# Kernel tuning notes

Measured on AMD Instinct MI355X. Metric: run time of the kernel, lower is better.

The kernel has to match this reference:

```python
import jax, jax.numpy as jnp
import numpy as np
import math

HEAD_DIM = 128

def _rope(t, cos, sin):
    # t: [B, S, H, D]; cos/sin: [S, D//2]; rotates consecutive pairs (view_as_complex semantics)
    B, S, H, D = t.shape
    t2 = t.reshape(B, S, H, D // 2, 2)
    t0, t1 = t2[..., 0], t2[..., 1]
    c = cos[None, :, None, :]
    s = sin[None, :, None, :]
    r0 = t0 * c - t1 * s
    r1 = t0 * s + t1 * c
    return jnp.stack([r0, r1], axis=-1).reshape(B, S, H, D)

def setup_inputs() -> dict:
    key = jax.random.key(0)
    ks = jax.random.split(key, 8)
    B, S, dim = 32, 1, 4096
    n_q, n_kv, hd = 32, 8, HEAD_DIM
    max_seq = 2048
    start_pos = 2047
    x = jax.random.normal(ks[0], (B, S, dim), dtype=jnp.float32)
    wq = jax.random.normal(ks[1], (n_q * hd, dim), dtype=jnp.float32) * 0.02
    wk = jax.random.normal(ks[2], (n_kv * hd, dim), dtype=jnp.float32) * 0.02
    wv = jax.random.normal(ks[3], (n_kv * hd, dim), dtype=jnp.float32) * 0.02
    wo = jax.random.normal(ks[4], (dim, n_q * hd), dtype=jnp.float32) * 0.02
    # real RoPE frequencies at positions [start_pos, start_pos+S)
    inv_freq = 1.0 / (10000.0 ** (np.arange(0, hd, 2, dtype=np.float32) / hd))  # [hd//2]
    pos = np.arange(start_pos, start_pos + S, dtype=np.float32)[:, None]
    angles = pos * inv_freq[None, :]  # [S, hd//2]
    freqs_cos = jnp.asarray(np.cos(angles), dtype=jnp.float32)
    freqs_sin = jnp.asarray(np.sin(angles), dtype=jnp.float32)
    cache_k = jax.random.normal(ks[5], (B, max_seq, n_kv, hd), dtype=jnp.float32)
    cache_v = jax.random.normal(ks[6], (B, max_seq, n_kv, hd), dtype=jnp.float32)
    return {"x": x, "wq": wq, "wk": wk, "wv": wv, "wo": wo,
            "freqs_cos": freqs_cos, "freqs_sin": freqs_sin,
            "cache_k": cache_k, "cache_v": cache_v, "start_pos": start_pos}

def reference(x, wq, wk, wv, wo, freqs_cos, freqs_sin, cache_k, cache_v, start_pos):
    B, S, dim = x.shape
    hd = HEAD_DIM
    n_q = wq.shape[0] // hd
    n_kv = wk.shape[0] // hd
    rep = n_q // n_kv
    q = (x @ wq.T).reshape(B, S, n_q, hd)
    k = (x @ wk.T).reshape(B, S, n_kv, hd)
    v = (x @ wv.T).reshape(B, S, n_kv, hd)
    q = _rope(q, freqs_cos, freqs_sin)
    k = _rope(k, freqs_cos, freqs_sin)
    # KV-cache update (start_pos is a static Python int)
    ck = jax.lax.dynamic_update_slice(cache_k, k, (0, start_pos, 0, 0))
    cv = jax.lax.dynamic_update_slice(cache_v, v, (0, start_pos, 0, 0))
    T = start_pos + S
    kk = ck[:, :T]  # [B, T, n_kv, hd]
    vv = cv[:, :T]
    # GQA without materializing repeated heads: q head h -> (g=h//rep, r=h%rep)
    qg = q.reshape(B, S, n_kv, rep, hd)
    scores = jnp.einsum('bsgrd,btgd->bgrst', qg, kk) / math.sqrt(hd)
    attn = jax.nn.softmax(scores, axis=-1)
    out = jnp.einsum('bgrst,btgd->bsgrd', attn, vv).reshape(B, S, n_q * hd)
    return out @ wo.T
```

## Files before the change

kernel.cpp:

```cpp
#include <hip/hip_runtime.h>
#include <hip/hip_bf16.h>


typedef __bf16 bf16x8_t __attribute__((ext_vector_type(8)));
typedef float f32x4_t __attribute__((ext_vector_type(4)));

#define KDIM 4096
#define NTOT_QKV 6144
#define NTOT_O 4096
#define NKV 8
#define HD 128

static __device__ inline bf16x8_t cvt8r(float4 u, float4 v) {
  bf16x8_t r;
  r[0] = (__bf16)u.x; r[1] = (__bf16)u.y; r[2] = (__bf16)u.z; r[3] = (__bf16)u.w;
  r[4] = (__bf16)v.x; r[5] = (__bf16)v.y; r[6] = (__bf16)v.z; r[7] = (__bf16)v.w;
  return r;
}

__global__ __launch_bounds__(256) void cast_x(const float* __restrict__ X,
                                              __bf16* __restrict__ Xb) {
  int i = blockIdx.x * 256 + threadIdx.x;
  const float4* p = (const float4*)(X + (size_t)i * 8);
  *(bf16x8_t*)(Xb + (size_t)i * 8) = cvt8r(p[0], p[1]);
}

__global__ __launch_bounds__(256) void qkv_mfma(
    const __bf16* __restrict__ Xb,
    const float* __restrict__ Wq,
    const float* __restrict__ Wk,
    const float* __restrict__ Wv,
    float* __restrict__ part)
{
  int nt = blockIdx.x % 96;
  int kc = blockIdx.x / 96;
  int k0 = kc << 9;
  int tid = threadIdx.x;
  int w = tid >> 6, lane = tid & 63;
  int rr = lane & 15, quad = lane >> 4;

  int ngbase = nt * 64;
  const float* Wbase;
  if (nt < 64)      Wbase = Wq + (size_t)ngbase * KDIM;
  else if (nt < 80) Wbase = Wk + (size_t)(ngbase - 4096) * KDIM;
  else              Wbase = Wv + (size_t)(ngbase - 5120) * KDIM;

  __shared__ bf16x8_t wl[2][512];

  int f8a = tid, f8b = tid + 256;
  int ra = f8a >> 3, ca = f8a & 7;
  int rb = f8b >> 3, cb = f8b & 7;
  const float4* ga = (const float4*)(Wbase + (size_t)ra * KDIM + k0 + ca * 8);
  const float4* gb = (const float4*)(Wbase + (size_t)rb * KDIM + k0 + cb * 8);
  int sa = ra * 8 + (ca ^ (ra & 7));
  int sb = rb * 8 + (cb ^ (rb & 7));

  const __bf16* xa0 = Xb + (size_t)rr * KDIM + k0 + quad * 8;
  const __bf16* xa1 = Xb + (size_t)(rr + 16) * KDIM + k0 + quad * 8;
  int brow = w * 16 + rr;
  int bs0 = brow * 8 + ((quad)     ^ (brow & 7));
  int bs1 = brow * 8 + ((quad + 4) ^ (brow & 7));

  f32x4_t acc0 = {0.f, 0.f, 0.f, 0.f};
  f32x4_t acc1 = {0.f, 0.f, 0.f, 0.f};

  float4 wa0 = ga[0], wa1 = ga[1], wb0 = gb[0], wb1 = gb[1];
  bf16x8_t A00 = *(const bf16x8_t*)(xa0);
  bf16x8_t A10 = *(const bf16x8_t*)(xa1);
  bf16x8_t A01 = *(const bf16x8_t*)(xa0 + 32);
  bf16x8_t A11 = *(const bf16x8_t*)(xa1 + 32);
  wl[0][sa] = cvt8r(wa0, wa1);
  wl[0][sb] = cvt8r(wb0, wb1);
  __syncthreads();

  #pragma unroll
  for (int s = 0; s < 8; ++s) {
    int cur = s & 1;
    float4 nwa0, nwa1, nwb0, nwb1;
    bf16x8_t N00, N10, N01, N11;
    if (s < 7) {
      nwa0 = ga[(s + 1) * 16];     nwa1 = ga[(s + 1) * 16 + 1];
      nwb0 = gb[(s + 1) * 16];     nwb1 = gb[(s + 1) * 16 + 1];
      N00 = *(const bf16x8_t*)(xa0 + (s + 1) * 64);
      N10 = *(const bf16x8_t*)(xa1 + (s + 1) * 64);
      N01 = *(const bf16x8_t*)(xa0 + (s + 1) * 64 + 32);
      N11 = *(const bf16x8_t*)(xa1 + (s + 1) * 64 + 32);
    }
    bf16x8_t b0 = wl[cur][bs0];
    bf16x8_t b1 = wl[cur][bs1];
    acc0 = __builtin_amdgcn_mfma_f32_16x16x32_bf16(A00, b0, acc0, 0, 0, 0);
    acc1 = __builtin_amdgcn_mfma_f32_16x16x32_bf16(A10, b0, acc1, 0, 0, 0);
    acc0 = __builtin_amdgcn_mfma_f32_16x16x32_bf16(A01, b1, acc0, 0, 0, 0);
    acc1 = __builtin_amdgcn_mfma_f32_16x16x32_bf16(A11, b1, acc1, 0, 0, 0);
    if (s < 7) {
      wl[cur ^ 1][sa] = cvt8r(nwa0, nwa1);
      wl[cur ^ 1][sb] = cvt8r(nwb0, nwb1);
      A00 = N00; A10 = N10; A01 = N01; A11 = N11;
    }
    __syncthreads();
  }

  int ng = ngbase + w * 16 + rr;
  float* p = part + (size_t)kc * 32 * NTOT_QKV + ng;
  #pragma unroll
  for (int i = 0; i < 4; ++i) {
    int m = quad * 4 + i;
    p[(size_t)m * NTOT_QKV] = acc0[i];
    p[(size_t)(m + 16) * NTOT_QKV] = acc1[i];
  }
}

__global__ __launch_bounds__(256) void reduce_rope(
    const float* __restrict__ part,
    const float* __restrict__ cosv,
    const float* __restrict__ sinv,
    float* __restrict__ qws,
    float* __restrict__ kws,
    float* __restrict__ vws)
{
  int idx = blockIdx.x * blockDim.x + threadIdx.x;
  int b = idx / 3072;
  int rem = idx - b * 3072;
  int n0 = rem * 2;
  const float* p = part + (size_t)b * NTOT_QKV + n0;
  float s0 = 0.f, s1 = 0.f;
  #pragma unroll
  for (int c = 0; c < 8; ++c) {
    s0 += p[(size_t)c * 32 * NTOT_QKV + 0];
    s1 += p[(size_t)c * 32 * NTOT_QKV + 1];
  }
  if (n0 < 4096) {
    int d = n0 & 127; int j = d >> 1;
    float cf = cosv[j], sf = sinv[j];
    qws[(size_t)b * 4096 + n0]     = s0 * cf - s1 * sf;
    qws[(size_t)b * 4096 + n0 + 1] = s0 * sf + s1 * cf;
  } else if (n0 < 5120) {
    int nn = n0 - 4096;
    int d = nn & 127; int j = d >> 1;
    float cf = cosv[j], sf = sinv[j];
    kws[(size_t)b * 1024 + nn]     = s0 * cf - s1 * sf;
    kws[(size_t)b * 1024 + nn + 1] = s0 * sf + s1 * cf;
  } else {
    int nn = n0 - 5120;
    vws[(size_t)b * 1024 + nn]     = s0;
    vws[(size_t)b * 1024 + nn + 1] = s1;
  }
}

__global__ __launch_bounds__(256) void attn_partial(
    const float* __restrict__ cache_k,
    const float* __restrict__ cache_v,
    const float* __restrict__ qws,
    const float* __restrict__ kws,
    const float* __restrict__ vws,
    float* __restrict__ part)
{
  int bidx = blockIdx.x;
  int c = bidx & 7;
  int pair = bidx >> 3;
  int h = pair & 7, b = pair >> 3;
  int tid = threadIdx.x;

  __shared__ float4 kbuf[2048];
  __shared__ float4 q4l[128];
  __shared__ float4 pl4[256];

  if (tid < 128)
    q4l[tid] = ((const float4*)(qws + (size_t)b * 4096 + (size_t)h * 512))[tid];

  const int r  = tid >> 6;
  const int tl = tid & 63;
  const int sw = tl & 7;

  const float* kcb = cache_k + (((size_t)b * 2048 + c * 256) * NKV + h) * HD;
  const float4* knew = (const float4*)(kws + ((size_t)b * NKV + h) * HD);

  float4 tmp[8];
  #pragma unroll
  for (int j = 0; j < 8; ++j) {
    int f = tid + j * 256, row = f >> 5, col = f & 31;
    tmp[j] = *((const float4*)(kcb + (size_t)row * (NKV * HD)) + col);
  }

  float s[4];
  #pragma unroll
  for (int st = 0; st < 4; ++st) {
    #pragma unroll
    for (int j = 0; j < 8; ++j) {
      int f = tid + j * 256;
      int row = f >> 5, col = f & 31;
      kbuf[row * 32 + (col ^ (row & 7))] = tmp[j];
    }
    __syncthreads();
    if (st < 3) {
      #pragma unroll
      for (int j = 0; j < 8; ++j) {
        int f = tid + j * 256, row = f >> 5, col = f & 31;
        const float4* src;
        if (c == 7 && st == 2 && row == 63)
          src = knew + col;
        else
          src = (const float4*)(kcb + (size_t)((st + 1) * 64 + row) * (NKV * HD)) + col;
        tmp[j] = *src;
      }
    }
    const float4* kr = kbuf + tl * 32;
    float acc = 0.f;
    #pragma unroll 8
    for (int d4 = 0; d4 < 32; ++d4) {
      float4 q4 = q4l[r * 32 + d4];
      float4 k4 = kr[d4 ^ sw];
      acc += q4.x * k4.x + q4.y * k4.y + q4.z * k4.z + q4.w * k4.w;
    }
    s[st] = acc * 0.088388347648318447f;
    __syncthreads();
  }

  float m = fmaxf(fmaxf(s[0], s[1]), fmaxf(s[2], s[3]));
  #pragma unroll
  for (int off = 32; off; off >>= 1) m = fmaxf(m, __shfl_xor(m, off, 64));
  float lsum = 0.f;
  float* plf = (float*)pl4;
  #pragma unroll
  for (int st = 0; st < 4; ++st) {
    float p = __expf(s[st] - m);
    lsum += p;
    plf[(st * 64 + tl) * 4 + r] = p;
  }
  #pragma unroll
  for (int off = 32; off; off >>= 1) lsum += __shfl_xor(lsum, off, 64);

  float* pb = part + (size_t)bidx * 520;
  if (tl == 0) { pb[r] = m; pb[4 + r] = lsum; }
  __syncthreads();

  int d4 = tid & 31;
  int g  = tid >> 5;
  float4 a0 = {0,0,0,0}, a1 = {0,0,0,0}, a2 = {0,0,0,0}, a3 = {0,0,0,0};
  const float4* vp = (const float4*)(cache_v +
      (((size_t)b * 2048 + c * 256 + g * 32) * NKV + h) * HD) + d4;
  #pragma unroll 4
  for (int i = 0; i < 32; ++i) {
    float4 v4 = vp[(size_t)i * 256];
    float4 pv = pl4[g * 32 + i];
    a0.x += pv.x * v4.x; a0.y += pv.x * v4.y; a0.z += pv.x * v4.z; a0.w += pv.x * v4.w;
    a1.x += pv.y * v4.x; a1.y += pv.y * v4.y; a1.z += pv.y * v4.z; a1.w += pv.y * v4.w;
    a2.x += pv.z * v4.x; a2.y += pv.z * v4.y; a2.z += pv.z * v4.z; a2.w += pv.z * v4.w;
    a3.x += pv.w * v4.x; a3.y += pv.w * v4.y; a3.z += pv.w * v4.z; a3.w += pv.w * v4.w;
  }
  if (c == 7 && g == 7) {
    float4 vold = vp[(size_t)31 * 256];
    float4 vn = ((const float4*)(vws + ((size_t)b * NKV + h) * HD))[d4];
    float4 dv; dv.x = vn.x - vold.x; dv.y = vn.y - vold.y;
    dv.z = vn.z - vold.z; dv.w = vn.w - vold.w;
    float4 pv = pl4[255];
    a0.x += pv.x * dv.x; a0.y += pv.x * dv.y; a0.z += pv.x * dv.z; a0.w += pv.x * dv.w;
    a1.x += pv.y * dv.x; a1.y += pv.y * dv.y; a1.z += pv.y * dv.z; a1.w += pv.y * dv.w;
    a2.x += pv.z * dv.x; a2.y += pv.z * dv.y; a2.z += pv.z * dv.z; a2.w += pv.z * dv.w;
    a3.x += pv.w * dv.x; a3.y += pv.w * dv.y; a3.z += pv.w * dv.z; a3.w += pv.w * dv.w;
  }
  float4* pred = kbuf;
  pred[(g * 4 + 0) * 32 + d4] = a0;
  pred[(g * 4 + 1) * 32 + d4] = a1;
  pred[(g * 4 + 2) * 32 + d4] = a2;
  pred[(g * 4 + 3) * 32 + d4] = a3;
  __syncthreads();

  if (tid < 128) {
    int r2 = tid >> 5, dd = tid & 31;
    float4 o = {0,0,0,0};
    #pragma unroll
    for (int gg = 0; gg < 8; ++gg) {
      float4 t4 = pred[(gg * 4 + r2) * 32 + dd];
      o.x += t4.x; o.y += t4.y; o.z += t4.z; o.w += t4.w;
    }
    *(float4*)(pb + 8 + r2 * 128 + dd * 4) = o;
  }
}

__global__ __launch_bounds__(128) void attn_combine(
    const float* __restrict__ part,
    __bf16* __restrict__ aobf)
{
  int pair = blockIdx.x;
  int h = pair & 7, b = pair >> 3;
  int d = threadIdx.x;
  const float* pb = part + (size_t)pair * 8 * 520;
  #pragma unroll
  for (int r = 0; r < 4; ++r) {
    float M = -1e30f;
    #pragma unroll
    for (int c = 0; c < 8; ++c) M = fmaxf(M, pb[c * 520 + r]);
    float L = 0.f, o = 0.f;
    #pragma unroll
    for (int c = 0; c < 8; ++c) {
      float w = __expf(pb[c * 520 + r] - M);
      L += w * pb[c * 520 + 4 + r];
      o += w * pb[c * 520 + 8 + r * 128 + d];
    }
    aobf[(size_t)b * 4096 + (h * 4 + r) * 128 + d] = (__bf16)(o / L);
  }
}

__global__ __launch_bounds__(256) void oproj_mfma(
    const __bf16* __restrict__ Xb,
    const float* __restrict__ W,
    float* __restrict__ part)
{
  int nt = blockIdx.x & 63;
  int kc = blockIdx.x >> 6;
  int k0 = kc << 9;
  int tid = threadIdx.x;
  int w = tid >> 6, lane = tid & 63;
  int rr = lane & 15, quad = lane >> 4;

  int ngbase = nt * 64;
  const float* Wbase = W + (size_t)ngbase * KDIM;

  __shared__ bf16x8_t wl[2][512];

  int f8a = tid, f8b = tid + 256;
  int ra = f8a >> 3, ca = f8a & 7;
  int rb = f8b >> 3, cb = f8b & 7;
  const float4* ga = (const float4*)(Wbase + (size_t)ra * KDIM + k0 + ca * 8);
  const float4* gb = (const float4*)(Wbase + (size_t)rb * KDIM + k0 + cb * 8);
  int sa = ra * 8 + (ca ^ (ra & 7));
  int sb = rb * 8 + (cb ^ (rb & 7));

  const __bf16* xa0 = Xb + (size_t)rr * KDIM + k0 + quad * 8;
  const __bf16* xa1 = Xb + (size_t)(rr + 16) * KDIM + k0 + quad * 8;
  int brow = w * 16 + rr;
  int bs0 = brow * 8 + ((quad)     ^ (brow & 7));
  int bs1 = brow * 8 + ((quad + 4) ^ (brow & 7));

  f32x4_t acc0 = {0.f, 0.f, 0.f, 0.f};
  f32x4_t acc1 = {0.f, 0.f, 0.f, 0.f};

  float4 wa0 = ga[0], wa1 = ga[1], wb0 = gb[0], wb1 = gb[1];
  bf16x8_t A00 = *(const bf16x8_t*)(xa0);
  bf16x8_t A10 = *(const bf16x8_t*)(xa1);
  bf16x8_t A01 = *(const bf16x8_t*)(xa0 + 32);
  bf16x8_t A11 = *(const bf16x8_t*)(xa1 + 32);
  wl[0][sa] = cvt8r(wa0, wa1);
  wl[0][sb] = cvt8r(wb0, wb1);
  __syncthreads();

  #pragma unroll
  for (int s = 0; s < 8; ++s) {
    int cur = s & 1;
    float4 nwa0, nwa1, nwb0, nwb1;
    bf16x8_t N00, N10, N01, N11;
    if (s < 7) {
      nwa0 = ga[(s + 1) * 16];     nwa1 = ga[(s + 1) * 16 + 1];
      nwb0 = gb[(s + 1) * 16];     nwb1 = gb[(s + 1) * 16 + 1];
      N00 = *(const bf16x8_t*)(xa0 + (s + 1) * 64);
      N10 = *(const bf16x8_t*)(xa1 + (s + 1) * 64);
      N01 = *(const bf16x8_t*)(xa0 + (s + 1) * 64 + 32);
      N11 = *(const bf16x8_t*)(xa1 + (s + 1) * 64 + 32);
    }
    bf16x8_t b0 = wl[cur][bs0];
    bf16x8_t b1 = wl[cur][bs1];
    acc0 = __builtin_amdgcn_mfma_f32_16x16x32_bf16(A00, b0, acc0, 0, 0, 0);
    acc1 = __builtin_amdgcn_mfma_f32_16x16x32_bf16(A10, b0, acc1, 0, 0, 0);
    acc0 = __builtin_amdgcn_mfma_f32_16x16x32_bf16(A01, b1, acc0, 0, 0, 0);
    acc1 = __builtin_amdgcn_mfma_f32_16x16x32_bf16(A11, b1, acc1, 0, 0, 0);
    if (s < 7) {
      wl[cur ^ 1][sa] = cvt8r(nwa0, nwa1);
      wl[cur ^ 1][sb] = cvt8r(nwb0, nwb1);
      A00 = N00; A10 = N10; A01 = N01; A11 = N11;
    }
    __syncthreads();
  }

  int ng = ngbase + w * 16 + rr;
  float* p = part + (size_t)kc * 32 * NTOT_O + ng;
  #pragma unroll
  for (int i = 0; i < 4; ++i) {
    int m = quad * 4 + i;
    p[(size_t)m * NTOT_O] = acc0[i];
    p[(size_t)(m + 16) * NTOT_O] = acc1[i];
  }
}

__global__ __launch_bounds__(256) void oproj_reduce(
    const float* __restrict__ part,
    float* __restrict__ out)
{
  int i = blockIdx.x * blockDim.x + threadIdx.x;
  float s = 0.f;
  #pragma unroll
  for (int c = 0; c < 8; ++c) s += part[(size_t)c * 131072 + i];
  out[i] = s;
}

extern "C" void kernel_launch(void* const* d_in, const int* in_sizes, int n_in,
                              void* d_out, int out_size, void* d_ws, size_t ws_size,
                              hipStream_t stream) {
  const float* x  = (const float*)d_in[0];
  const float* wq = (const float*)d_in[1];
  const float* wk = (const float*)d_in[2];
  const float* wv = (const float*)d_in[3];
  const float* wo = (const float*)d_in[4];
  const float* fc = (const float*)d_in[5];
  const float* fs = (const float*)d_in[6];
  const float* ck = (const float*)d_in[7];
  const float* cv = (const float*)d_in[8];

  char* ws = (char*)d_ws;
  float*  part_qkv = (float*)(ws + 0);
  float*  qws      = (float*)(ws + 6291456);
  float*  kws      = (float*)(ws + 6815744);
  float*  vws      = (float*)(ws + 6946816);
  float*  part_at  = (float*)(ws + 7077888);
  __bf16* xbf      = (__bf16*)(ws + 11337728);
  __bf16* aobf     = (__bf16*)(ws + 11599872);
  float*  part_o   = (float*)(ws + 0);

  cast_x<<<64, 256, 0, stream>>>(x, xbf);
  qkv_mfma<<<768, 256, 0, stream>>>(xbf, wq, wk, wv, part_qkv);
  reduce_rope<<<384, 256, 0, stream>>>(part_qkv, fc, fs, qws, kws, vws);
  attn_partial<<<2048, 256, 0, stream>>>(ck, cv, qws, kws, vws, part_at);
  attn_combine<<<256, 128, 0, stream>>>(part_at, aobf);
  oproj_mfma<<<512, 256, 0, stream>>>(aobf, wo, part_o);
  oproj_reduce<<<512, 256, 0, stream>>>(part_o, (float*)d_out);
}
```

Baseline: 678.3 us.

## Compute attention scores straight from global K, dropping LDS K staging

The QK^T phase no longer stages 256 K rows through a 32KB shared buffer with double-buffered register prefetch and barriers. Each group of 4 lanes now reads one K row directly from global memory and reduces partial dots with shuffles, with q held in registers. Shared memory drops to about 20KB and launch bounds request 4 blocks per CU, aiming for more occupancy and no barriers in the score loop. The cost is that each of the 4 warps reads the same K rows redundantly, relying on cache for reuse, and every lane redoes the exp, so the row sum is scaled by 0.25.

Measured after the change: 678.6 us. About the same (+0.1%).

```diff
diff --git a/kernel.cpp b/kernel.cpp
--- a/kernel.cpp
+++ b/kernel.cpp
@@ -147,7 +147,7 @@
   }
 }
 
-__global__ __launch_bounds__(256) void attn_partial(
+__global__ __launch_bounds__(256, 4) void attn_partial(
     const float* __restrict__ cache_k,
     const float* __restrict__ cache_v,
     const float* __restrict__ qws,
@@ -161,74 +161,57 @@
   int h = pair & 7, b = pair >> 3;
   int tid = threadIdx.x;
 
-  __shared__ float4 kbuf[2048];
-  __shared__ float4 q4l[128];
-  __shared__ float4 pl4[256];
-
-  if (tid < 128)
-    q4l[tid] = ((const float4*)(qws + (size_t)b * 4096 + (size_t)h * 512))[tid];
+  __shared__ float plf[4 * 256];
+  __shared__ float4 pred[1024];
 
   const int r  = tid >> 6;
   const int tl = tid & 63;
-  const int sw = tl & 7;
+  const int tq = tl >> 2;
+  const int dq = tl & 3;
+
+  const float4* Q4 = (const float4*)(qws + (size_t)b * 4096 + (size_t)h * 512) + r * 32;
+  float4 q4[8];
+  #pragma unroll
+  for (int i = 0; i < 8; ++i) q4[i] = Q4[dq + 4 * i];
 
   const float* kcb = cache_k + (((size_t)b * 2048 + c * 256) * NKV + h) * HD;
   const float4* knew = (const float4*)(kws + ((size_t)b * NKV + h) * HD);
 
-  float4 tmp[8];
-  #pragma unroll
-  for (int j = 0; j < 8; ++j) {
-    int f = tid + j * 256, row = f >> 5, col = f & 31;
-    tmp[j] = *((const float4*)(kcb + (size_t)row * (NKV * HD)) + col);
-  }
-
-  float s[4];
-  #pragma unroll
-  for (int st = 0; st < 4; ++st) {
+  float sreg[16];
+  #pragma unroll
+  for (int ps = 0; ps < 16; ++ps) {
+    int trow = ps * 16 + tq;
+    const float4* kp = (c == 7 && trow == 255)
+        ? knew
+        : (const float4*)(kcb + (size_t)trow * (NKV * HD));
+    float acc = 0.f;
     #pragma unroll
-    for (int j = 0; j < 8; ++j) {
-      int f = tid + j * 256;
-      int row = f >> 5, col = f & 31;
-      kbuf[row * 32 + (col ^ (row & 7))] = tmp[j];
-    }
-    __syncthreads();
-    if (st < 3) {
-      #pragma unroll
-      for (int j = 0; j < 8; ++j) {
-        int f = tid + j * 256, row = f >> 5, col = f & 31;
-        const float4* src;
-        if (c == 7 && st == 2 && row == 63)
-          src = knew + col;
-        else
-          src = (const float4*)(kcb + (size_t)((st + 1) * 64 + row) * (NKV * HD)) + col;
-        tmp[j] = *src;
-      }
-    }
-    const float4* kr = kbuf + tl * 32;
-    float acc = 0.f;
-    #pragma unroll 8
-    for (int d4 = 0; d4 < 32; ++d4) {
-      float4 q4 = q4l[r * 32 + d4];
-      float4 k4 = kr[d4 ^ sw];
-      acc += q4.x * k4.x + q4.y * k4.y + q4.z * k4.z + q4.w * k4.w;
-    }
-    s[st] = acc * 0.088388347648318447f;
-    __syncthreads();
-  }
-
-  float m = fmaxf(fmaxf(s[0], s[1]), fmaxf(s[2], s[3]));
+    for (int i = 0; i < 8; ++i) {
+      float4 k4 = kp[dq + 4 * i];
+      float4 qq = q4[i];
+      acc += qq.x * k4.x + qq.y * k4.y + qq.z * k4.z + qq.w * k4.w;
+    }
+    acc += __shfl_xor(acc, 1, 64);
+    acc += __shfl_xor(acc, 2, 64);
+    sreg[ps] = acc * 0.088388347648318447f;
+  }
+
+  float m = sreg[0];
+  #pragma unroll
+  for (int ps = 1; ps < 16; ++ps) m = fmaxf(m, sreg[ps]);
   #pragma unroll
   for (int off = 32; off; off >>= 1) m = fmaxf(m, __shfl_xor(m, off, 64));
+
   float lsum = 0.f;
-  float* plf = (float*)pl4;
-  #pragma unroll
-  for (int st = 0; st < 4; ++st) {
-    float p = __expf(s[st] - m);
+  #pragma unroll
+  for (int ps = 0; ps < 16; ++ps) {
+    float p = __expf(sreg[ps] - m);
     lsum += p;
-    plf[(st * 64 + tl) * 4 + r] = p;
+    if (dq == 0) plf[r * 256 + ps * 16 + tq] = p;
   }
   #pragma unroll
   for (int off = 32; off; off >>= 1) lsum += __shfl_xor(lsum, off, 64);
+  lsum *= 0.25f;
 
   float* pb = part + (size_t)bidx * 520;
   if (tl == 0) { pb[r] = m; pb[4 + r] = lsum; }
@@ -242,24 +225,30 @@
   #pragma unroll 4
   for (int i = 0; i < 32; ++i) {
     float4 v4 = vp[(size_t)i * 256];
-    float4 pv = pl4[g * 32 + i];
-    a0.x += pv.x * v4.x; a0.y += pv.x * v4.y; a0.z += pv.x * v4.z; a0.w += pv.x * v4.w;
-    a1.x += pv.y * v4.x; a1.y += pv.y * v4.y; a1.z += pv.y * v4.z; a1.w += pv.y * v4.w;
-    a2.x += pv.z * v4.x; a2.y += pv.z * v4.y; a2.z += pv.z * v4.z; a2.w += pv.z * v4.w;
-    a3.x += pv.w * v4.x; a3.y += pv.w * v4.y; a3.z += pv.w * v4.z; a3.w += pv.w * v4.w;
+    int t = g * 32 + i;
+    float p0 = plf[t];
+    float p1 = plf[256 + t];
+    float p2 = plf[512 + t];
+    float p3 = plf[768 + t];
+    a0.x += p0 * v4.x; a0.y += p0 * v4.y; a0.z += p0 * v4.z; a0.w += p0 * v4.w;
+    a1.x += p1 * v4.x; a1.y += p1 * v4.y; a1.z += p1 * v4.z; a1.w += p1 * v4.w;
+    a2.x += p2 * v4.x; a2.y += p2 * v4.y; a2.z += p2 * v4.z; a2.w += p2 * v4.w;
+    a3.x += p3 * v4.x; a3.y += p3 * v4.y; a3.z += p3 * v4.z; a3.w += p3 * v4.w;
   }
   if (c == 7 && g == 7) {
     float4 vold = vp[(size_t)31 * 256];
     float4 vn = ((const float4*)(vws + ((size_t)b * NKV + h) * HD))[d4];
     float4 dv; dv.x = vn.x - vold.x; dv.y = vn.y - vold.y;
     dv.z = vn.z - vold.z; dv.w = vn.w - vold.w;
-    float4 pv = pl4[255];
-    a0.x += pv.x * dv.x; a0.y += pv.x * dv.y; a0.z += pv.x * dv.z; a0.w += pv.x * dv.w;
-    a1.x += pv.y * dv.x; a1.y += pv.y * dv.y; a1.z += pv.y * dv.z; a1.w += pv.y * dv.w;
-    a2.x += pv.z * dv.x; a2.y += pv.z * dv.y; a2.z += pv.z * dv.z; a2.w += pv.z * dv.w;
-    a3.x += pv.w * dv.x; a3.y += pv.w * dv.y; a3.z += pv.w * dv.z; a3.w += pv.w * dv.w;
-  }
-  float4* pred = kbuf;
+    float p0 = plf[255];
+    float p1 = plf[256 + 255];
+    float p2 = plf[512 + 255];
+    float p3 = plf[768 + 255];
+    a0.x += p0 * dv.x; a0.y += p0 * dv.y; a0.z += p0 * dv.z; a0.w += p0 * dv.w;
+    a1.x += p1 * dv.x; a1.y += p1 * dv.y; a1.z += p1 * dv.z; a1.w += p1 * dv.w;
+    a2.x += p2 * dv.x; a2.y += p2 * dv.y; a2.z += p2 * dv.z; a2.w += p2 * dv.w;
+    a3.x += p3 * dv.x; a3.y += p3 * dv.y; a3.z += p3 * dv.z; a3.w += p3 * dv.w;
+  }
   pred[(g * 4 + 0) * 32 + d4] = a0;
   pred[(g * 4 + 1) * 32 + d4] = a1;
   pred[(g * 4 + 2) * 32 + d4] = a2;
```
